# Performance work log

Hardware: AMD Instinct MI355X
Metric: run time of the kernel (lower is better)

Reference implementation:

```python
import jax, jax.numpy as jnp
import numpy as np

B, C, L, H = 4, 128, 4096, 4
GROUPS, EPS = 32, 1e-5


def group_norm(x, gamma, beta):
    # x: [B, C, L]; normalize per (batch, group) over (C//G, L)
    b, c, l = x.shape
    xg = x.reshape(b, GROUPS, c // GROUPS, l)
    mu = jnp.mean(xg, axis=(2, 3), keepdims=True)
    var = jnp.var(xg, axis=(2, 3), keepdims=True)
    xn = ((xg - mu) * jax.lax.rsqrt(var + EPS)).reshape(b, c, l)
    return xn * gamma[None, :, None] + beta[None, :, None]


def setup_inputs() -> dict:
    key = jax.random.key(0)
    k1, k2, k3 = jax.random.split(key, 3)
    return {
        "x": jax.random.normal(k1, (B, C, L), dtype=jnp.float32),
        "w_qkv": jax.random.normal(k2, (3 * C, C), dtype=jnp.float32) * 0.02,
        "w_proj": jax.random.normal(k3, (C, C), dtype=jnp.float32) * 0.02,
        "b_proj": jnp.zeros((C,), dtype=jnp.float32),
        "gn_gamma": jnp.ones((C,), dtype=jnp.float32),
        "gn_beta": jnp.zeros((C,), dtype=jnp.float32),
    }


def reference(x, w_qkv, w_proj, b_proj, gn_gamma, gn_beta):
    b, c, l = x.shape
    hd = c // H
    h = group_norm(x, gn_gamma, gn_beta)
    # 1x1 conv == channel matmul: [B, 3C, L]
    qkv = jnp.einsum('oc,bcl->bol', w_qkv, h)
    # torch reshape(B*H, 3C/H, L).chunk(3, dim=1): per-head contiguous slices
    qkv = qkv.reshape(b, H, 3 * hd, l)
    q, k, v = qkv[:, :, :hd], qkv[:, :, hd:2 * hd], qkv[:, :, 2 * hd:]
    scale = 1.0 / np.sqrt(np.sqrt(hd)).astype(np.float32)
    attn = jnp.einsum('bhct,bhcs->bhts', q * scale, k * scale)
    attn = jax.nn.softmax(attn, axis=-1)
    o = jnp.einsum('bhts,bhcs->bhct', attn, v).reshape(b, c, l)
    o = jnp.einsum('oc,bcl->bol', w_proj, o) + b_proj[None, :, None]
    return o + x
```

## Files before the change

kernel.cpp:

```cpp
#include <hip/hip_runtime.h>
#include <hip/hip_bf16.h>
#include <cstdint>
#include <cstddef>


#define B_ 4
#define C_ 128
#define L_ 4096
#define H_ 4
#define HD_ 32
#define NG_ 32
#define CPG_ 4
#define EPS_ 1e-5f
#define QKSCALE_ 0.5050097650430367f

typedef __attribute__((ext_vector_type(8))) short bf16x8;
typedef __attribute__((ext_vector_type(8))) unsigned short u16x8;
typedef __attribute__((ext_vector_type(4))) float f32x4;
typedef __attribute__((ext_vector_type(16))) float f32x16;
typedef __attribute__((ext_vector_type(2))) _Float16 f16x2;
typedef __attribute__((ext_vector_type(4))) _Float16 f16x4;
typedef __attribute__((ext_vector_type(8))) _Float16 f16x8;
typedef __attribute__((ext_vector_type(2))) unsigned int u32x2;
typedef __attribute__((ext_vector_type(4))) unsigned int u32x4;

#if __has_builtin(__builtin_amdgcn_exp2f)
#define EXP2F(x) __builtin_amdgcn_exp2f(x)
#else
#define EXP2F(x) exp2f(x)
#endif

__device__ __forceinline__ float bu2f(unsigned short u) {
  return __builtin_bit_cast(float, (unsigned int)(((unsigned int)u) << 16));
}
__device__ __forceinline__ unsigned short f2bu(float f) {
  unsigned int u = __builtin_bit_cast(unsigned int, f);
  unsigned int r = (u + 0x7fffu + ((u >> 16) & 1u)) >> 16;
  return (unsigned short)r;
}
__device__ __forceinline__ float4 u42f4(ushort4 u) {
  return make_float4(bu2f(u.x), bu2f(u.y), bu2f(u.z), bu2f(u.w));
}
__device__ __forceinline__ unsigned int pkbf(float a, float b) {
  return (unsigned int)f2bu(a) | ((unsigned int)f2bu(b) << 16);
}
__device__ __forceinline__ f16x2 pkhf2(float a, float b) {
#if __has_builtin(__builtin_amdgcn_cvt_pkrtz)
  return __builtin_bit_cast(f16x2, __builtin_amdgcn_cvt_pkrtz(a, b));
#else
  f16x2 r;
  r[0] = (_Float16)a;
  r[1] = (_Float16)b;
  return r;
#endif
}
__device__ __forceinline__ unsigned int pkhf(float a, float b) {
  return __builtin_bit_cast(unsigned int, pkhf2(a, b));
}

__device__ __forceinline__ void gload16(const void* g, void* l) {
  __builtin_amdgcn_global_load_lds(
      (const __attribute__((address_space(1))) unsigned int*)g,
      (__attribute__((address_space(3))) unsigned int*)l, 16, 0, 0);
}

__device__ __forceinline__ bool detect_fast(const ushort* x) {
  __shared__ int flag_s;
  int t = threadIdx.x;
  if (t < 64) {
    int e = (x[t] >> 7) & 0xFF;
    unsigned long long m = __ballot((e < 64) || (e > 192));
    if (t == 0) flag_s = (__popcll(m) > 4) ? 1 : 0;
  }
  __syncthreads();
  return flag_s != 0;
}

__device__ __forceinline__ float4 ldx4(const void* x, size_t idx, bool f32) {
  if (f32) return *((const float4*)x + (idx >> 2));
  ushort4 u = *((const ushort4*)x + (idx >> 2));
  return u42f4(u);
}

__global__ __launch_bounds__(256) void gn_stats(const void* __restrict__ x,
                                                const void* __restrict__ wq,
                                                const void* __restrict__ wp,
                                                const void* __restrict__ bp,
                                                const void* __restrict__ gm,
                                                const void* __restrict__ bt,
                                                ushort* __restrict__ wq_b,
                                                ushort* __restrict__ wp_b,
                                                float* __restrict__ bp_f,
                                                float2* __restrict__ gn_ab) {
  bool f32 = detect_fast((const ushort*)x);
  int blk = blockIdx.x;
  int t = threadIdx.x;

  if (blk >= 128) {
    int i0 = ((blk - 128) * 256 + t) * 8;
#pragma unroll
    for (int k = 0; k < 8; ++k) {
      int i = i0 + k;
      if (i >= 65664) break;
      if (i < 49152) {
        wq_b[i] = f32 ? f2bu(((const float*)wq)[i]) : ((const ushort*)wq)[i];
      } else if (i < 65536) {
        int off = i - 49152;
        wp_b[off] = f32 ? f2bu(((const float*)wp)[off]) : ((const ushort*)wp)[off];
      } else {
        int off = i - 65536;
        bp_f[off] = f32 ? ((const float*)bp)[off] : bu2f(((const ushort*)bp)[off]);
      }
    }
    return;
  }

  int b = blk >> 5, g = blk & 31;
  size_t base = ((size_t)b * C_ + (size_t)g * CPG_) * L_;

  float s = 0.f, ss = 0.f;
#pragma unroll
  for (int i = 0; i < 16; ++i) {
    size_t e = base + i * 1024 + t * 4;
    float4 f = ldx4(x, e, f32);
    s += f.x + f.y + f.z + f.w;
    ss += f.x * f.x + f.y * f.y + f.z * f.z + f.w * f.w;
  }
#pragma unroll
  for (int m = 32; m >= 1; m >>= 1) {
    s += __shfl_xor(s, m, 64);
    ss += __shfl_xor(ss, m, 64);
  }
  __shared__ float red[4][2];
  int wv = t >> 6;
  if ((t & 63) == 0) { red[wv][0] = s; red[wv][1] = ss; }
  __syncthreads();
  float ts = red[0][0] + red[1][0] + red[2][0] + red[3][0];
  float tss = red[0][1] + red[1][1] + red[2][1] + red[3][1];
  float mu = ts * (1.0f / 16384.0f);
  float var = tss * (1.0f / 16384.0f) - mu * mu;
  float rs = rsqrtf(var + EPS_);

  if (t < CPG_) {
    int gi = g * CPG_ + t;
    float ga = f32 ? ((const float*)gm)[gi] : bu2f(((const ushort*)gm)[gi]);
    float be = f32 ? ((const float*)bt)[gi] : bu2f(((const ushort*)bt)[gi]);
    gn_ab[b * C_ + gi] = make_float2(ga * rs, be - mu * ga * rs);
  }
}

__global__ __launch_bounds__(256) void qkv_kernel(const ushort* __restrict__ wq_b,
                                                  const void* __restrict__ x,
                                                  const float2* __restrict__ gn_ab,
                                                  ushort* __restrict__ Qt,
                                                  ushort* __restrict__ Kt,
                                                  ushort* __restrict__ Vb) {
  bool f32 = detect_fast((const ushort*)x);
  __shared__ alignas(16) ushort Hs[64][136];
  __shared__ alignas(16) float Ls[64][69];

  int lx = blockIdx.x, oz = blockIdx.y, b = blockIdx.z;
  int t = threadIdx.x;
  int w = t >> 6, lane = t & 63, l16 = lane & 15, q = lane >> 4, q8 = q * 8;

  {
    int u = t & 63, lh = (t >> 6) * 16;
    int c0 = 2 * u;
    float2 ab0 = gn_ab[b * C_ + c0];
    float2 ab1 = gn_ab[b * C_ + c0 + 1];
    size_t xo = ((size_t)b * C_ + c0) * L_ + (size_t)lx * 64 + lh;
#pragma unroll
    for (int j = 0; j < 4; ++j) {
      float4 f0 = ldx4(x, xo + j * 4, f32);
      float4 f1 = ldx4(x, xo + L_ + j * 4, f32);
      float n0[4] = {f0.x * ab0.x + ab0.y, f0.y * ab0.x + ab0.y,
                     f0.z * ab0.x + ab0.y, f0.w * ab0.x + ab0.y};
      float n1[4] = {f1.x * ab1.x + ab1.y, f1.y * ab1.x + ab1.y,
                     f1.z * ab1.x + ab1.y, f1.w * ab1.x + ab1.y};
#pragma unroll
      for (int k = 0; k < 4; ++k)
        *(unsigned int*)&Hs[lh + j * 4 + k][c0] = pkbf(n0[k], n1[k]);
    }
  }
  __syncthreads();

  for (int j = 0; j < 2; ++j) {
    int oy = oz * 2 + j;
    const ushort* wg = wq_b + (size_t)(oy * 64 + w * 16 + l16) * C_;

    f32x4 acc[4] = {{0.f, 0.f, 0.f, 0.f}, {0.f, 0.f, 0.f, 0.f},
                    {0.f, 0.f, 0.f, 0.f}, {0.f, 0.f, 0.f, 0.f}};
#pragma unroll
    for (int kc = 0; kc < 4; ++kc) {
      bf16x8 aw = *(const bf16x8*)(wg + kc * 32 + q8);
#pragma unroll
      for (int nb = 0; nb < 4; ++nb) {
        bf16x8 bh = *(const bf16x8*)&Hs[nb * 16 + l16][kc * 32 + q8];
        acc[nb] = __builtin_amdgcn_mfma_f32_16x16x32_bf16(aw, bh, acc[nb], 0, 0, 0);
      }
    }
    __syncthreads();
#pragma unroll
    for (int nb = 0; nb < 4; ++nb)
#pragma unroll
      for (int r = 0; r < 4; ++r)
        Ls[nb * 16 + l16][w * 16 + 4 * q + r] = acc[nb][r];
    __syncthreads();

#pragma unroll
    for (int hhalf = 0; hhalf < 2; ++hhalf) {
      int hh = oy * 2 + hhalf;
      int type = hh % 3, head = hh / 3;
      size_t bh = (size_t)b * H_ + head;
      if (type == 2) {
        int c_loc = t >> 3, l8 = (t & 7) * 8;
        float v[8];
#pragma unroll
        for (int jj = 0; jj < 8; ++jj) v[jj] = Ls[l8 + jj][hhalf * 32 + c_loc];
        uint4 u;
        u.x = pkhf(v[0], v[1]);
        u.y = pkhf(v[2], v[3]);
        u.z = pkhf(v[4], v[5]);
        u.w = pkhf(v[6], v[7]);
        *(uint4*)(Vb + (bh * 32 + c_loc) * L_ + (size_t)lx * 64 + l8) = u;
      } else {
        ushort* dst = type ? Kt : Qt;
        int l = t >> 2, seg = (t & 3) * 8;
        const float* src = &Ls[l][hhalf * 32 + seg];
        uint4 u;
        u.x = pkbf(src[0] * QKSCALE_, src[1] * QKSCALE_);
        u.y = pkbf(src[2] * QKSCALE_, src[3] * QKSCALE_);
        u.z = pkbf(src[4] * QKSCALE_, src[5] * QKSCALE_);
        u.w = pkbf(src[6] * QKSCALE_, src[7] * QKSCALE_);
        *(uint4*)(dst + ((bh * L_) + lx * 64 + l) * 32 + seg) = u;
      }
    }
  }
}

__global__ __launch_bounds__(512, 6) void attn_kernel(const ushort* __restrict__ Qt,
                                                      const ushort* __restrict__ Kt,
                                                      const ushort* __restrict__ Vb,
                                                      ushort* __restrict__ ot) {
  __shared__ alignas(16) char smem[35840];

  int t = threadIdx.x;
  int w = t >> 6, lane = t & 63, l31 = lane & 31, hi = lane >> 5;
  int qt = w & 3, sh = w >> 2;
  int tq0 = blockIdx.x * 128;
  int bh = blockIdx.y;
  int b = bh >> 2, head = bh & 3;
  const ushort* Qg = Qt + ((size_t)bh * L_ + tq0) * 32;
  const ushort* Kg = Kt + (size_t)bh * L_ * 32;
  const ushort* Vg = Vb + (size_t)bh * 32 * L_;

  int rd = t >> 2, pd = t & 3;
  int kcsem = (pd - rd) & 3;
  const ushort* ksrc = Kg + (size_t)rd * 32 + kcsem * 8;
  int vr = t >> 4, vp = t & 15;
  int vcsem = (vp & 8) | ((vp & 7) ^ (vr & 7));
  const ushort* vsrc = Vg + (size_t)vr * L_ + vcsem * 8;

  char* kb0 = smem;
  char* kb1 = smem + 8192;
  char* vb0 = smem + 16384;
  char* vb1 = smem + 24576;

  const ushort* qbase = Qg + (size_t)(qt * 32 + l31) * 32;
  bf16x8 qB0 = *(const bf16x8*)(qbase + 8 * hi);
  bf16x8 qB1 = *(const bf16x8*)(qbase + 16 + 8 * hi);

  const f16x2 one2 = {(_Float16)1.0f, (_Float16)1.0f};

  gload16(ksrc, kb0 + (size_t)t * 16);
  gload16(vsrc, vb0 + (size_t)t * 16);
  ksrc += 4096;
  vsrc += 128;
  __syncthreads();

  f32x16 aO = {0.f};
  float lsum = 0.f;

  int flip = 0;
  for (int it = 0; it < 32; ++it) {
    if (it < 31) {
      gload16(ksrc, (flip ? kb0 : kb1) + (size_t)t * 16);
      gload16(vsrc, (flip ? vb0 : vb1) + (size_t)t * 16);
      ksrc += 4096;
      vsrc += 128;
    }
    const ushort* kc = (const ushort*)(flip ? kb1 : kb0);
    const ushort* vc = (const ushort*)(flip ? vb1 : vb0);

#pragma unroll
    for (int st = 0; st < 2; ++st) {
      int s0 = 64 * sh + 32 * st;
      const ushort* krow = kc + (size_t)(s0 + l31) * 32;
      bf16x8 aK0 = *(const bf16x8*)(krow + ((hi + l31) & 3) * 8);
      bf16x8 aK1 = *(const bf16x8*)(krow + ((2 + hi + l31) & 3) * 8);
      f32x16 zz = {0.f};
      f32x16 sf;
      __builtin_amdgcn_s_setprio(1);
      sf = __builtin_amdgcn_mfma_f32_32x32x16_bf16(aK0, qB0, zz, 0, 0, 0);
      sf = __builtin_amdgcn_mfma_f32_32x32x16_bf16(aK1, qB1, sf, 0, 0, 0);
      __builtin_amdgcn_s_setprio(0);

#pragma unroll
      for (int sb = 0; sb < 2; ++sb) {
        int sblk = 4 * sh + 2 * st + sb;
        int kci = 2 * sblk + hi;
        int vpos = (kci & 8) | ((kci & 7) ^ (l31 & 7));
        f16x8 vf = *(const f16x8*)(vc + (size_t)l31 * 128 + vpos * 8);

        float p0 = EXP2F(sf[8 * sb + 0]);
        float p1 = EXP2F(sf[8 * sb + 1]);
        float p2 = EXP2F(sf[8 * sb + 2]);
        float p3 = EXP2F(sf[8 * sb + 3]);
        float p4 = EXP2F(sf[8 * sb + 4]);
        float p5 = EXP2F(sf[8 * sb + 5]);
        float p6 = EXP2F(sf[8 * sb + 6]);
        float p7 = EXP2F(sf[8 * sb + 7]);
        f16x2 cA0 = pkhf2(p0, p1), cA1 = pkhf2(p2, p3);
        f16x2 cB0 = pkhf2(p4, p5), cB1 = pkhf2(p6, p7);
        lsum = __builtin_amdgcn_fdot2(cA0, one2, lsum, false);
        lsum = __builtin_amdgcn_fdot2(cA1, one2, lsum, false);
        lsum = __builtin_amdgcn_fdot2(cB0, one2, lsum, false);
        lsum = __builtin_amdgcn_fdot2(cB1, one2, lsum, false);

        u32x2 r0 = __builtin_amdgcn_permlane32_swap(
            __builtin_bit_cast(unsigned int, cA0),
            __builtin_bit_cast(unsigned int, cB0), false, false);
        u32x2 r1 = __builtin_amdgcn_permlane32_swap(
            __builtin_bit_cast(unsigned int, cA1),
            __builtin_bit_cast(unsigned int, cB1), false, false);
        u32x4 pw = {r0.x, r1.x, r0.y, r1.y};
        f16x8 pf = __builtin_bit_cast(f16x8, pw);

        __builtin_amdgcn_s_setprio(1);
        aO = __builtin_amdgcn_mfma_f32_32x32x16_f16(vf, pf, aO, 0, 0, 0);
        __builtin_amdgcn_s_setprio(0);
      }
    }
    __syncthreads();
    flip ^= 1;
  }

  float* Osh = (float*)smem;
  float* Lp = (float*)(smem + 33792);
  {
    float* ob = Osh + (size_t)(sh * 4 + qt) * (32 * 33) + (size_t)l31 * 33;
#pragma unroll
    for (int reg = 0; reg < 16; ++reg) {
      int R = (reg & 3) + 8 * (reg >> 2) + 4 * hi;
      ob[R] = aO[reg];
    }
    Lp[(sh * 2 + hi) * 128 + qt * 32 + l31] = lsum;
  }
  __syncthreads();

  {
    int qloc = t >> 2, c0 = (t & 3) * 8;
    int qt2 = qloc >> 5, q31 = qloc & 31;
    float lt = Lp[qloc] + Lp[128 + qloc] + Lp[256 + qloc] + Lp[384 + qloc];
    float inv = 1.0f / lt;
    const float* o0 = Osh + (size_t)qt2 * (32 * 33) + (size_t)q31 * 33 + c0;
    const float* o1 = o0 + 4 * (32 * 33);
    float o[8];
#pragma unroll
    for (int jj = 0; jj < 8; ++jj) o[jj] = (o0[jj] + o1[jj]) * inv;
    uint4 u;
    u.x = pkbf(o[0], o[1]);
    u.y = pkbf(o[2], o[3]);
    u.z = pkbf(o[4], o[5]);
    u.w = pkbf(o[6], o[7]);
    *(uint4*)(ot + ((size_t)b * L_ + tq0 + qloc) * C_ + head * 32 + c0) = u;
  }
}

__global__ __launch_bounds__(256) void proj_kernel(const ushort* __restrict__ wp_b,
                                                   const float* __restrict__ bias,
                                                   const void* __restrict__ x,
                                                   const ushort* __restrict__ ot,
                                                   void* __restrict__ out) {
  bool f32 = detect_fast((const ushort*)x);
  __shared__ alignas(16) float Ls[64][37];

  int lx = blockIdx.x, oy = blockIdx.y, b = blockIdx.z;
  int t = threadIdx.x;
  int w = t >> 6, lane = t & 63, l16 = lane & 15, q = lane >> 4, q8 = q * 8;

  const ushort* wg = wp_b + (size_t)(oy * 64 + w * 16 + l16) * C_;
  const ushort* og = ot + ((size_t)b * L_ + (size_t)lx * 32) * C_;

  f32x4 acc[2] = {{0.f, 0.f, 0.f, 0.f}, {0.f, 0.f, 0.f, 0.f}};
#pragma unroll
  for (int kc = 0; kc < 4; ++kc) {
    bf16x8 aw = *(const bf16x8*)(wg + kc * 32 + q8);
#pragma unroll
    for (int nb = 0; nb < 2; ++nb) {
      bf16x8 bo = *(const bf16x8*)(og + (size_t)(nb * 16 + l16) * C_ + kc * 32 + q8);
      acc[nb] = __builtin_amdgcn_mfma_f32_16x16x32_bf16(aw, bo, acc[nb], 0, 0, 0);
    }
  }
#pragma unroll
  for (int nb = 0; nb < 2; ++nb)
#pragma unroll
    for (int r = 0; r < 4; ++r)
      Ls[w * 16 + 4 * q + r][nb * 16 + l16] = acc[nb][r];
  __syncthreads();

  {
    int o_loc = t >> 2, ls0 = (t & 3) * 8;
    float bv = bias[oy * 64 + o_loc];
    size_t off = ((size_t)b * C_ + oy * 64 + o_loc) * L_ + (size_t)lx * 32 + ls0;
#pragma unroll
    for (int jj = 0; jj < 2; ++jj) {
      float4 xf = ldx4(x, off + jj * 4, f32);
      const float* sp = &Ls[o_loc][ls0 + jj * 4];
      float4 r = make_float4(sp[0] + bv + xf.x, sp[1] + bv + xf.y,
                             sp[2] + bv + xf.z, sp[3] + bv + xf.w);
      if (f32) {
        *(float4*)((float*)out + off + jj * 4) = r;
      } else {
        *(ushort4*)((ushort*)out + off + jj * 4) =
            make_ushort4(f2bu(r.x), f2bu(r.y), f2bu(r.z), f2bu(r.w));
      }
    }
  }
}

extern "C" void kernel_launch(void* const* d_in, const int* in_sizes, int n_in,
                              void* d_out, int out_size, void* d_ws, size_t ws_size,
                              hipStream_t stream) {
  const void* x      = d_in[0];
  const void* w_qkv  = d_in[1];
  const void* w_proj = d_in[2];
  const void* b_proj = d_in[3];
  const void* gamma  = d_in[4];
  const void* beta   = d_in[5];

  char* wsb = (char*)d_ws;
  ushort* wq_b  = (ushort*)(wsb + 0);
  ushort* wp_b  = (ushort*)(wsb + 98304);
  float*  bp_f  = (float*)(wsb + 131072);
  float2* gn_ab = (float2*)(wsb + 131584);
  ushort* Qt    = (ushort*)(wsb + 8388608);
  ushort* Kt    = (ushort*)(wsb + 12582912);
  ushort* Vb    = (ushort*)(wsb + 16777216);
  ushort* ot    = (ushort*)(wsb + 20971520);

  gn_stats<<<dim3(161), dim3(256), 0, stream>>>(x, w_qkv, w_proj, b_proj, gamma, beta,
                                                wq_b, wp_b, bp_f, gn_ab);
  qkv_kernel<<<dim3(L_ / 64, 3, B_), dim3(256), 0, stream>>>(wq_b, x, gn_ab, Qt, Kt, Vb);
  attn_kernel<<<dim3(L_ / 128, B_ * H_), dim3(512), 0, stream>>>(Qt, Kt, Vb, ot);
  proj_kernel<<<dim3(L_ / 32, C_ / 64, B_), dim3(256), 0, stream>>>(wp_b, bp_f, x, ot, d_out);
}
```

Measured before the change: 138.5 us.

## Split attention over two key halves with a combine kernel; split GN stats

The attention kernel now splits the key/value sequence into two halves on a new grid dimension. Each half writes unnormalized fp32 partial outputs and row sums, and a new combine kernel adds them, normalizes and packs to bf16. This doubles the number of attention blocks to fill more CUs (launch bounds raised to 8 waves), at the cost of extra fp32 partial traffic and one more launch. Group-norm statistics are also split across twice as many blocks, with the final mean/rstd computed inside the qkv kernel.

```diff
diff --git a/kernel.cpp b/kernel.cpp
--- a/kernel.cpp
+++ b/kernel.cpp
@@ -86,18 +86,16 @@
                                                 const void* __restrict__ wq,
                                                 const void* __restrict__ wp,
                                                 const void* __restrict__ bp,
-                                                const void* __restrict__ gm,
-                                                const void* __restrict__ bt,
                                                 ushort* __restrict__ wq_b,
                                                 ushort* __restrict__ wp_b,
                                                 float* __restrict__ bp_f,
-                                                float2* __restrict__ gn_ab) {
+                                                float2* __restrict__ gpart) {
   bool f32 = detect_fast((const ushort*)x);
   int blk = blockIdx.x;
   int t = threadIdx.x;
 
-  if (blk >= 128) {
-    int i0 = ((blk - 128) * 256 + t) * 8;
+  if (blk >= 256) {
+    int i0 = ((blk - 256) * 256 + t) * 8;
 #pragma unroll
     for (int k = 0; k < 8; ++k) {
       int i = i0 + k;
@@ -115,16 +113,20 @@
     return;
   }
 
-  int b = blk >> 5, g = blk & 31;
-  size_t base = ((size_t)b * C_ + (size_t)g * CPG_) * L_;
+  int b = blk >> 6, rem = blk & 63;
+  int g = rem >> 1, half = rem & 1;
+  size_t base = ((size_t)b * C_ + (size_t)g * CPG_) * L_ + (size_t)half * 2048;
 
   float s = 0.f, ss = 0.f;
 #pragma unroll
-  for (int i = 0; i < 16; ++i) {
-    size_t e = base + i * 1024 + t * 4;
-    float4 f = ldx4(x, e, f32);
-    s += f.x + f.y + f.z + f.w;
-    ss += f.x * f.x + f.y * f.y + f.z * f.z + f.w * f.w;
+  for (int cc = 0; cc < 4; ++cc) {
+#pragma unroll
+    for (int i = 0; i < 2; ++i) {
+      size_t e = base + (size_t)cc * L_ + i * 1024 + t * 4;
+      float4 f = ldx4(x, e, f32);
+      s += f.x + f.y + f.z + f.w;
+      ss += f.x * f.x + f.y * f.y + f.z * f.z + f.w * f.w;
+    }
   }
 #pragma unroll
   for (int m = 32; m >= 1; m >>= 1) {
@@ -135,39 +137,52 @@
   int wv = t >> 6;
   if ((t & 63) == 0) { red[wv][0] = s; red[wv][1] = ss; }
   __syncthreads();
-  float ts = red[0][0] + red[1][0] + red[2][0] + red[3][0];
-  float tss = red[0][1] + red[1][1] + red[2][1] + red[3][1];
-  float mu = ts * (1.0f / 16384.0f);
-  float var = tss * (1.0f / 16384.0f) - mu * mu;
-  float rs = rsqrtf(var + EPS_);
-
-  if (t < CPG_) {
-    int gi = g * CPG_ + t;
-    float ga = f32 ? ((const float*)gm)[gi] : bu2f(((const ushort*)gm)[gi]);
-    float be = f32 ? ((const float*)bt)[gi] : bu2f(((const ushort*)bt)[gi]);
-    gn_ab[b * C_ + gi] = make_float2(ga * rs, be - mu * ga * rs);
+  if (t == 0) {
+    float ts = red[0][0] + red[1][0] + red[2][0] + red[3][0];
+    float tss = red[0][1] + red[1][1] + red[2][1] + red[3][1];
+    gpart[(b * 32 + g) * 2 + half] = make_float2(ts, tss);
   }
 }
 
 __global__ __launch_bounds__(256) void qkv_kernel(const ushort* __restrict__ wq_b,
                                                   const void* __restrict__ x,
-                                                  const float2* __restrict__ gn_ab,
+                                                  const float2* __restrict__ gpart,
+                                                  const void* __restrict__ gm,
+                                                  const void* __restrict__ bt,
                                                   ushort* __restrict__ Qt,
                                                   ushort* __restrict__ Kt,
                                                   ushort* __restrict__ Vb) {
   bool f32 = detect_fast((const ushort*)x);
   __shared__ alignas(16) ushort Hs[64][136];
   __shared__ alignas(16) float Ls[64][69];
+  __shared__ float2 abs_s[128];
 
   int lx = blockIdx.x, oz = blockIdx.y, b = blockIdx.z;
   int t = threadIdx.x;
   int w = t >> 6, lane = t & 63, l16 = lane & 15, q = lane >> 4, q8 = q * 8;
 
+  if (t < 64) {
+#pragma unroll
+    for (int k = 0; k < 2; ++k) {
+      int c = 2 * t + k;
+      int g = c >> 2;
+      float2 p0 = gpart[(b * 32 + g) * 2];
+      float2 p1 = gpart[(b * 32 + g) * 2 + 1];
+      float mu = (p0.x + p1.x) * (1.0f / 16384.0f);
+      float var = (p0.y + p1.y) * (1.0f / 16384.0f) - mu * mu;
+      float rs = rsqrtf(var + EPS_);
+      float ga = f32 ? ((const float*)gm)[c] : bu2f(((const ushort*)gm)[c]);
+      float be = f32 ? ((const float*)bt)[c] : bu2f(((const ushort*)bt)[c]);
+      abs_s[c] = make_float2(ga * rs, be - mu * ga * rs);
+    }
+  }
+  __syncthreads();
+
   {
     int u = t & 63, lh = (t >> 6) * 16;
     int c0 = 2 * u;
-    float2 ab0 = gn_ab[b * C_ + c0];
-    float2 ab1 = gn_ab[b * C_ + c0 + 1];
+    float2 ab0 = abs_s[c0];
+    float2 ab1 = abs_s[c0 + 1];
     size_t xo = ((size_t)b * C_ + c0) * L_ + (size_t)lx * 64 + lh;
 #pragma unroll
     for (int j = 0; j < 4; ++j) {
@@ -238,21 +253,23 @@
   }
 }
 
-__global__ __launch_bounds__(512, 6) void attn_kernel(const ushort* __restrict__ Qt,
+__global__ __launch_bounds__(512, 8) void attn_kernel(const ushort* __restrict__ Qt,
                                                       const ushort* __restrict__ Kt,
                                                       const ushort* __restrict__ Vb,
-                                                      ushort* __restrict__ ot) {
+                                                      float* __restrict__ Po,
+                                                      float* __restrict__ Lg) {
   __shared__ alignas(16) char smem[35840];
 
   int t = threadIdx.x;
   int w = t >> 6, lane = t & 63, l31 = lane & 31, hi = lane >> 5;
   int qt = w & 3, sh = w >> 2;
   int tq0 = blockIdx.x * 128;
-  int bh = blockIdx.y;
+  int ss = blockIdx.y;
+  int bh = blockIdx.z;
   int b = bh >> 2, head = bh & 3;
   const ushort* Qg = Qt + ((size_t)bh * L_ + tq0) * 32;
-  const ushort* Kg = Kt + (size_t)bh * L_ * 32;
-  const ushort* Vg = Vb + (size_t)bh * 32 * L_;
+  const ushort* Kg = Kt + ((size_t)bh * L_ + (size_t)ss * 2048) * 32;
+  const ushort* Vg = Vb + (size_t)bh * 32 * L_ + (size_t)ss * 2048;
 
   int rd = t >> 2, pd = t & 3;
   int kcsem = (pd - rd) & 3;
@@ -282,8 +299,8 @@
   float lsum = 0.f;
 
   int flip = 0;
-  for (int it = 0; it < 32; ++it) {
-    if (it < 31) {
+  for (int it = 0; it < 16; ++it) {
+    if (it < 15) {
       gload16(ksrc, (flip ? kb0 : kb1) + (size_t)t * 16);
       gload16(vsrc, (flip ? vb0 : vb1) + (size_t)t * 16);
       ksrc += 4096;
@@ -362,19 +379,43 @@
     int qloc = t >> 2, c0 = (t & 3) * 8;
     int qt2 = qloc >> 5, q31 = qloc & 31;
     float lt = Lp[qloc] + Lp[128 + qloc] + Lp[256 + qloc] + Lp[384 + qloc];
-    float inv = 1.0f / lt;
     const float* o0 = Osh + (size_t)qt2 * (32 * 33) + (size_t)q31 * 33 + c0;
     const float* o1 = o0 + 4 * (32 * 33);
     float o[8];
 #pragma unroll
-    for (int jj = 0; jj < 8; ++jj) o[jj] = (o0[jj] + o1[jj]) * inv;
-    uint4 u;
-    u.x = pkbf(o[0], o[1]);
-    u.y = pkbf(o[2], o[3]);
-    u.z = pkbf(o[4], o[5]);
-    u.w = pkbf(o[6], o[7]);
-    *(uint4*)(ot + ((size_t)b * L_ + tq0 + qloc) * C_ + head * 32 + c0) = u;
-  }
+    for (int jj = 0; jj < 8; ++jj) o[jj] = o0[jj] + o1[jj];
+    float* dst = Po + (size_t)ss * ((size_t)B_ * L_ * C_) +
+                 ((size_t)b * L_ + tq0 + qloc) * C_ + head * 32 + c0;
+    *(float4*)dst = make_float4(o[0], o[1], o[2], o[3]);
+    *(float4*)(dst + 4) = make_float4(o[4], o[5], o[6], o[7]);
+    if ((t & 3) == 0) Lg[((size_t)ss * 16 + bh) * L_ + tq0 + qloc] = lt;
+  }
+}
+
+__global__ __launch_bounds__(256) void combine_kernel(const float* __restrict__ Po,
+                                                      const float* __restrict__ Lg,
+                                                      ushort* __restrict__ ot) {
+  int tl = blockIdx.x * 256 + threadIdx.x;
+  int row = tl >> 4;
+  int c0 = (tl & 15) * 8;
+  int head = c0 >> 5;
+  int b = row >> 12, l = row & 4095;
+  const size_t HALF = (size_t)B_ * L_ * C_;
+  const float* p0 = Po + (size_t)row * C_ + c0;
+  const float* p1 = p0 + HALF;
+  float lv = Lg[(size_t)(b * 4 + head) * L_ + l] +
+             Lg[(size_t)(16 + b * 4 + head) * L_ + l];
+  float inv = 1.0f / lv;
+  float4 a0 = *(const float4*)p0;
+  float4 a1 = *(const float4*)(p0 + 4);
+  float4 b0 = *(const float4*)p1;
+  float4 b1 = *(const float4*)(p1 + 4);
+  uint4 u;
+  u.x = pkbf((a0.x + b0.x) * inv, (a0.y + b0.y) * inv);
+  u.y = pkbf((a0.z + b0.z) * inv, (a0.w + b0.w) * inv);
+  u.z = pkbf((a1.x + b1.x) * inv, (a1.y + b1.y) * inv);
+  u.w = pkbf((a1.z + b1.z) * inv, (a1.w + b1.w) * inv);
+  *(uint4*)(ot + (size_t)row * C_ + c0) = u;
 }
 
 __global__ __launch_bounds__(256) void proj_kernel(const ushort* __restrict__ wp_b,
@@ -443,15 +484,19 @@
   ushort* wq_b  = (ushort*)(wsb + 0);
   ushort* wp_b  = (ushort*)(wsb + 98304);
   float*  bp_f  = (float*)(wsb + 131072);
-  float2* gn_ab = (float2*)(wsb + 131584);
+  float2* gpart = (float2*)(wsb + 131584);
+  float*  Lg    = (float*)(wsb + 139264);
   ushort* Qt    = (ushort*)(wsb + 8388608);
+  ushort* ot    = (ushort*)(wsb + 8388608);
   ushort* Kt    = (ushort*)(wsb + 12582912);
   ushort* Vb    = (ushort*)(wsb + 16777216);
-  ushort* ot    = (ushort*)(wsb + 20971520);
-
-  gn_stats<<<dim3(161), dim3(256), 0, stream>>>(x, w_qkv, w_proj, b_proj, gamma, beta,
-                                                wq_b, wp_b, bp_f, gn_ab);
-  qkv_kernel<<<dim3(L_ / 64, 3, B_), dim3(256), 0, stream>>>(wq_b, x, gn_ab, Qt, Kt, Vb);
-  attn_kernel<<<dim3(L_ / 128, B_ * H_), dim3(512), 0, stream>>>(Qt, Kt, Vb, ot);
+  float*  Po    = (float*)(wsb + 20971520);
+
+  gn_stats<<<dim3(289), dim3(256), 0, stream>>>(x, w_qkv, w_proj, b_proj,
+                                                wq_b, wp_b, bp_f, gpart);
+  qkv_kernel<<<dim3(L_ / 64, 3, B_), dim3(256), 0, stream>>>(wq_b, x, gpart, gamma, beta,
+                                                             Qt, Kt, Vb);
+  attn_kernel<<<dim3(L_ / 128, 2, B_ * H_), dim3(512), 0, stream>>>(Qt, Kt, Vb, Po, Lg);
+  combine_kernel<<<dim3(1024), dim3(256), 0, stream>>>(Po, Lg, ot);
   proj_kernel<<<dim3(L_ / 32, C_ / 64, B_), dim3(256), 0, stream>>>(wp_b, bp_f, x, ot, d_out);
 }
```

New measurement: 146.6 us. 1.06x slower.
